# Optimization experiments

Hardware: AMD Instinct MI355X
Metric: run time of the kernel (lower is better)

Reference implementation:

```python
import jax, jax.numpy as jnp
import numpy as np

BITS = 8
NUM_HEADS = 16
EMB = 1024
MLP = 4096
BATCH = 4
SEQ = 1024


def _fq(x, bits, signed=True, narrow=False):
    """Fake-quantize with per-tensor absmax scale (brevitas MinMax/MaxStats style),
    straight-through-estimator round. signed+narrow => weight quant; signed non-narrow
    => activation quant; unsigned => QuantReLU output."""
    if signed:
        qmax = 2.0 ** (bits - 1) - 1.0
        qmin = -qmax if narrow else -(qmax + 1.0)
    else:
        qmax = 2.0 ** bits - 1.0
        qmin = 0.0
    scale = jax.lax.stop_gradient(jnp.max(jnp.abs(x)) / qmax)
    scale = jnp.maximum(scale, jnp.asarray(1e-8, x.dtype))
    q = x / scale
    q = q + jax.lax.stop_gradient(jnp.round(q) - q)  # STE round
    return jnp.clip(q, qmin, qmax) * scale


def _layernorm(x, eps=1e-5):
    mu = jnp.mean(x, axis=-1, keepdims=True)
    var = jnp.mean(jnp.square(x - mu), axis=-1, keepdims=True)
    return (x - mu) * jax.lax.rsqrt(var + eps)


def setup_inputs() -> dict:
    key = jax.random.key(0)
    ks = jax.random.split(key, 11)
    def w(k, shape, fan_in):
        return jax.random.normal(k, shape, jnp.float32) * (1.0 / np.sqrt(fan_in))
    return {
        "x": jax.random.normal(ks[0], (BATCH, SEQ, EMB), jnp.float32),
        "Wq": w(ks[1], (EMB, EMB), EMB), "bq": jnp.zeros((EMB,), jnp.float32),
        "Wk": w(ks[2], (EMB, EMB), EMB), "bk": jnp.zeros((EMB,), jnp.float32),
        "Wv": w(ks[3], (EMB, EMB), EMB), "bv": jnp.zeros((EMB,), jnp.float32),
        "Wo": w(ks[4], (EMB, EMB), EMB), "bo": jnp.zeros((EMB,), jnp.float32),
        "W1": w(ks[5], (MLP, EMB), EMB), "b1": jnp.zeros((MLP,), jnp.float32),
        "W2": w(ks[6], (EMB, MLP), MLP), "b2": jnp.zeros((EMB,), jnp.float32),
    }


def reference(x, Wq, bq, Wk, bk, Wv, bv, Wo, bo, W1, b1, W2, b2):
    B, S, E = x.shape
    H, D = NUM_HEADS, EMB // NUM_HEADS
    fqw = lambda W: _fq(W, BITS, signed=True, narrow=True)   # weight quant
    fqb = lambda b: _fq(b, BITS, signed=True)                # bias quant
    fqa = lambda a: _fq(a, BITS, signed=True)                # act quant

    # sdp_input_quant
    qx = fqa(x)
    # separate (unpacked) in-projections, torch Linear: y = x @ W.T + b
    q = qx @ fqw(Wq).T + fqb(bq)
    k = qx @ fqw(Wk).T + fqb(bk)
    v = qx @ fqw(Wv).T + fqb(bv)
    # [B,H,S,D]
    q = q.reshape(B, S, H, D).transpose(0, 2, 1, 3)
    k = k.reshape(B, S, H, D).transpose(0, 2, 1, 3)
    v = v.reshape(B, S, H, D).transpose(0, 2, 1, 3)

    q_scaled = fqa(q * (1.0 / np.sqrt(D)))          # q_scaled_quant
    k_t = fqa(k.transpose(0, 1, 3, 2))              # k_transposed_quant
    v = fqa(v)                                      # v_quant

    scores = jnp.einsum('bhqd,bhdk->bhqk', q_scaled, k_t)
    scores = fqa(scores)                            # softmax_input_quant
    attn = jax.nn.softmax(scores, axis=-1)
    attn = fqa(attn)                                # attn_output_weights_quant

    ctx = jnp.einsum('bhqk,bhkd->bhqd', attn, v)
    ctx = ctx.transpose(0, 2, 1, 3).reshape(B, S, E)
    ctx = fqa(ctx)                                  # out_proj_input_quant
    attn_out = ctx @ fqw(Wo).T + fqb(bo)

    # residual_sdp (QuantEltwiseAdd input quant on both operands) + layer-norm
    h = _layernorm(fqa(x) + fqa(attn_out))

    # MLP: QuantIdentity -> QuantLinear -> QuantReLU(unsigned) -> QuantLinear
    m = fqa(h)
    m = m @ fqw(W1).T + fqb(b1)
    m = _fq(jax.nn.relu(m), BITS, signed=False)
    m = m @ fqw(W2).T + fqb(b2)

    return _layernorm(fqa(h) + fqa(m))
```

## Files before the change

### kernel.cpp

```cpp
#include <hip/hip_runtime.h>
#include <cstdint>
#include <cstddef>

#define TB_B 4
#define TB_S 1024
#define TB_E 1024
#define TB_H 16
#define TB_D 64
#define TB_MLP 4096
#define TB_ROWS (TB_B * TB_S)

typedef int int4v __attribute__((ext_vector_type(4)));

#define LGKM0() __asm__ volatile("s_waitcnt lgkmcnt(0)" ::: "memory")
#define CMEMBAR() __asm__ volatile("" ::: "memory")

static __device__ __forceinline__ void atomicMaxF(float* addr, float v) {
  atomicMax(reinterpret_cast<unsigned int*>(addr), __float_as_uint(v));
}

static __device__ __forceinline__ float fast_exp2(float x) {
#if __has_builtin(__builtin_amdgcn_exp2f)
  return __builtin_amdgcn_exp2f(x);
#else
  return exp2f(x);
#endif
}

static __device__ __forceinline__ void gl2lds16(const void* g, void* l) {
  __builtin_amdgcn_global_load_lds(
      (const __attribute__((address_space(1))) void*)g,
      (__attribute__((address_space(3))) void*)l, 16, 0, 0);
}

struct AMDesc { const float* p; long n4; int slot; };
struct AMBatch { AMDesc d[13]; };
__global__ __launch_bounds__(256) void absmax_multi_kernel(AMBatch bt, float* ws) {
  AMDesc d = bt.d[blockIdx.y];
  float m = 0.f;
  long stride = (long)gridDim.x * 256;
  for (long i = (long)blockIdx.x * 256 + threadIdx.x; i < d.n4; i += stride) {
    float4 v = ((const float4*)d.p)[i];
    m = fmaxf(m, fmaxf(fmaxf(fabsf(v.x), fabsf(v.y)), fmaxf(fabsf(v.z), fabsf(v.w))));
  }
#pragma unroll
  for (int o = 32; o; o >>= 1) m = fmaxf(m, __shfl_down(m, o, 64));
  __shared__ float sm[4];
  if (!(threadIdx.x & 63)) sm[threadIdx.x >> 6] = m;
  __syncthreads();
  if (threadIdx.x == 0)
    atomicMaxF(ws + d.slot, fmaxf(fmaxf(sm[0], sm[1]), fmaxf(sm[2], sm[3])));
}

struct QMDesc { const float* in; signed char* out; long n4; int slot; float qmin; };
struct QMBatch { QMDesc d[7]; };
__global__ __launch_bounds__(256) void quant8_multi_kernel(QMBatch bt, const float* ws) {
  QMDesc d = bt.d[blockIdx.y];
  float scale = fmaxf(ws[d.slot] / 127.f, 1e-8f);
  long stride = (long)gridDim.x * 256;
  for (long i = (long)blockIdx.x * 256 + threadIdx.x; i < d.n4; i += stride) {
    float4 v = ((const float4*)d.in)[i];
    char4 o;
    o.x = (signed char)(int)fminf(fmaxf(rintf(v.x / scale), d.qmin), 127.f);
    o.y = (signed char)(int)fminf(fmaxf(rintf(v.y / scale), d.qmin), 127.f);
    o.z = (signed char)(int)fminf(fmaxf(rintf(v.z / scale), d.qmin), 127.f);
    o.w = (signed char)(int)fminf(fmaxf(rintf(v.w / scale), d.qmin), 127.f);
    ((char4*)d.out)[i] = o;
  }
}

struct BDesc { const float* in; float* out; int n4; int slot; };
struct BBatch { BDesc d[6]; };
__global__ __launch_bounds__(256) void bias_quant_multi_kernel(BBatch bt, const float* ws) {
  BDesc d = bt.d[blockIdx.y];
  float scale = fmaxf(ws[d.slot] / 127.f, 1e-8f);
  int i = blockIdx.x * 256 + threadIdx.x;
  if (i < d.n4) {
    float4 v = ((const float4*)d.in)[i];
    float4 o;
    o.x = fminf(fmaxf(rintf(v.x / scale), -128.f), 127.f) * scale;
    o.y = fminf(fmaxf(rintf(v.y / scale), -128.f), 127.f) * scale;
    o.z = fminf(fmaxf(rintf(v.z / scale), -128.f), 127.f) * scale;
    o.w = fminf(fmaxf(rintf(v.w / scale), -128.f), 127.f) * scale;
    ((float4*)d.out)[i] = o;
  }
}

__global__ __launch_bounds__(256) void quant8_kernel(const float* __restrict__ in,
                                                     signed char* __restrict__ out8, long n4,
                                                     const float* __restrict__ amax_p,
                                                     float pre, float qmin) {
  float scale = fmaxf(amax_p[0] * pre / 127.f, 1e-8f);
  long stride = (long)gridDim.x * 256;
  for (long i = (long)blockIdx.x * 256 + threadIdx.x; i < n4; i += stride) {
    float4 v = ((const float4*)in)[i];
    char4 o;
    o.x = (signed char)(int)fminf(fmaxf(rintf(v.x * pre / scale), qmin), 127.f);
    o.y = (signed char)(int)fminf(fmaxf(rintf(v.y * pre / scale), qmin), 127.f);
    o.z = (signed char)(int)fminf(fmaxf(rintf(v.z * pre / scale), qmin), 127.f);
    o.w = (signed char)(int)fminf(fmaxf(rintf(v.w * pre / scale), qmin), 127.f);
    ((char4*)out8)[i] = o;
  }
}

__global__ __launch_bounds__(256) void relu_quant8_kernel(const float* __restrict__ in,
                                                          signed char* __restrict__ out8, long n4,
                                                          const float* __restrict__ amax_p) {
  float scale = fmaxf(amax_p[0] / 255.f, 1e-8f);
  long stride = (long)gridDim.x * 256;
  for (long i = (long)blockIdx.x * 256 + threadIdx.x; i < n4; i += stride) {
    float4 v = ((const float4*)in)[i];
    char4 o;
    o.x = (signed char)((int)fminf(fmaxf(rintf(fmaxf(v.x, 0.f) / scale), 0.f), 255.f) - 128);
    o.y = (signed char)((int)fminf(fmaxf(rintf(fmaxf(v.y, 0.f) / scale), 0.f), 255.f) - 128);
    o.z = (signed char)((int)fminf(fmaxf(rintf(fmaxf(v.z, 0.f) / scale), 0.f), 255.f) - 128);
    o.w = (signed char)((int)fminf(fmaxf(rintf(fmaxf(v.w, 0.f) / scale), 0.f), 255.f) - 128);
    ((char4*)out8)[i] = o;
  }
}

__global__ __launch_bounds__(256) void rowsum_i8_kernel(const signed char* __restrict__ w8,
                                                        int* __restrict__ out, int Kdim) {
  const int row = blockIdx.x, t = threadIdx.x;
  const signed char* p = w8 + (long)row * Kdim;
  int s = 0;
  for (int i = t * 16; i < Kdim; i += 4096) {
    int4v v = *(const int4v*)(p + i);
    const signed char* b = (const signed char*)&v;
#pragma unroll
    for (int j = 0; j < 16; j++) s += b[j];
  }
#pragma unroll
  for (int o = 32; o; o >>= 1) s += __shfl_down(s, o, 64);
  __shared__ int sm[4];
  if (!(t & 63)) sm[t >> 6] = s;
  __syncthreads();
  if (t == 0) out[row] = sm[0] + sm[1] + sm[2] + sm[3];
}

__global__ __launch_bounds__(256) void gemm_i8_kernel(
    const signed char* __restrict__ A, const signed char* __restrict__ Bw,
    const float* __restrict__ biasq,
    const float* __restrict__ amax_a, float div_a,
    const float* __restrict__ amax_b,
    const int* __restrict__ rowsum,
    float* __restrict__ C, int M, int N, int K,
    float* __restrict__ amax_out, int relu_amax, int mode) {
  __shared__ signed char As[2][8192];
  __shared__ signed char Bs[2][8192];
  const int t = threadIdx.x;
  int bx, by;
  {
    int lin = blockIdx.y * gridDim.x + blockIdx.x;
    if ((gridDim.y & 7) == 0) {
      int xcd = lin & 7, j = lin >> 3;
      bx = j % gridDim.x;
      by = (gridDim.y >> 3) * xcd + j / gridDim.x;
    } else { bx = blockIdx.x; by = blockIdx.y; }
  }
  const int m0 = by * 128, n0 = bx * 128;
  const int w = t >> 6, lane = t & 63;
  const int fr = lane & 15, quad = lane >> 4;
  const int wm = w >> 1, wn = w & 1;
  const int r0 = t >> 2;
  const int csrc = (((t & 3) ^ ((t >> 3) & 3)) << 4);
  const int sx = ((quad ^ ((fr >> 1) & 3)) << 4);

  int4v acc[4][4];
#pragma unroll
  for (int r = 0; r < 4; r++)
#pragma unroll
    for (int c = 0; c < 4; c++) acc[r][c] = (int4v){0, 0, 0, 0};

  const long arow0 = (long)(m0 + r0) * K + csrc;
  const long arow1 = (long)(m0 + r0 + 64) * K + csrc;
  const long brow0 = (long)(n0 + r0) * K + csrc;
  const long brow1 = (long)(n0 + r0 + 64) * K + csrc;

  auto stage = [&](int buf, int kk) {
    gl2lds16(A + arow0 + kk, As[buf] + t * 16);
    gl2lds16(A + arow1 + kk, As[buf] + t * 16 + 4096);
    gl2lds16(Bw + brow0 + kk, Bs[buf] + t * 16);
    gl2lds16(Bw + brow1 + kk, Bs[buf] + t * 16 + 4096);
  };
  auto compute = [&](int buf) {
    int4v af[4], bf[4];
#pragma unroll
    for (int r = 0; r < 4; r++)
      af[r] = *(const int4v*)(As[buf] + (wm * 64 + r * 16 + fr) * 64 + sx);
#pragma unroll
    for (int c = 0; c < 4; c++)
      bf[c] = *(const int4v*)(Bs[buf] + (wn * 64 + c * 16 + fr) * 64 + sx);
#pragma unroll
    for (int r = 0; r < 4; r++)
#pragma unroll
      for (int c = 0; c < 4; c++)
        acc[r][c] = __builtin_amdgcn_mfma_i32_16x16x64_i8(af[r], bf[c], acc[r][c], 0, 0, 0);
  };

  const int nt = K >> 6;
  stage(0, 0);
  __syncthreads();
  for (int kt = 0; kt < nt; kt += 2) {
    stage(1, (kt + 1) << 6);
    compute(0);
    __syncthreads();
    if (kt + 2 < nt) stage(0, (kt + 2) << 6);
    compute(1);
    __syncthreads();
  }

  const int seg = (mode == 1) ? (n0 >> 10) : 0;
  const float s_a = fmaxf(amax_a[0] / div_a, 1e-8f);
  const float s_b = fmaxf(amax_b[seg] / 127.f, 1e-8f);
  const float s = s_a * s_b;
  float lmax = 0.f;
#pragma unroll
  for (int r = 0; r < 4; r++) {
    int rbase = m0 + wm * 64 + r * 16 + quad * 4;
#pragma unroll
    for (int c = 0; c < 4; c++) {
      int col = n0 + wn * 64 + c * 16 + fr;
      int corr = rowsum ? (rowsum[col] << 7) : 0;
      float bi = biasq[col];
      if (mode == 1) {
        int h = (col >> 6) & 15, dd = col & 63;
        float* cbase = C + (long)seg * ((long)TB_ROWS * TB_E);
#pragma unroll
        for (int g = 0; g < 4; g++) {
          int m = rbase + g;
          int b = m >> 10, sdx = m & 1023;
          float o = (float)acc[r][c][g] * s + bi;
          lmax = fmaxf(lmax, fabsf(o));
          cbase[((((long)b * TB_H + h) * TB_S) + sdx) * TB_D + dd] = o;
        }
      } else {
#pragma unroll
        for (int g = 0; g < 4; g++) {
          float o = (float)(acc[r][c][g] + corr) * s + bi;
          lmax = fmaxf(lmax, relu_amax ? fmaxf(o, 0.f) : fabsf(o));
          C[(long)(rbase + g) * N + col] = o;
        }
      }
    }
  }
#pragma unroll
  for (int o = 32; o; o >>= 1) lmax = fmaxf(lmax, __shfl_down(lmax, o, 64));
  __shared__ float redm[4];
  if (!lane) redm[w] = lmax;
  __syncthreads();
  if (t == 0) atomicMaxF(amax_out + seg, fmaxf(fmaxf(redm[0], redm[1]), fmaxf(redm[2], redm[3])));
}

__global__ __launch_bounds__(256) void quant8_vb_kernel(const float* __restrict__ v,
                                                        const float* __restrict__ amax_p,
                                                        signed char* __restrict__ v8b) {
  __shared__ signed char tile[64][80];
  const int bh = blockIdx.x;
  const int jb = blockIdx.y;
  const int s0 = jb * 64;
  const int t = threadIdx.x;
  const float scale = fmaxf(amax_p[0] / 127.f, 1e-8f);
#pragma unroll
  for (int it = 0; it < 4; it++) {
    int idx = t + it * 256;
    int r = idx >> 4, c4 = (idx & 15) * 4;
    float4 vv = *(const float4*)(v + ((long)bh * TB_S + s0 + r) * TB_D + c4);
    tile[c4 + 0][r] = (signed char)(int)fminf(fmaxf(rintf(vv.x / scale), -128.f), 127.f);
    tile[c4 + 1][r] = (signed char)(int)fminf(fmaxf(rintf(vv.y / scale), -128.f), 127.f);
    tile[c4 + 2][r] = (signed char)(int)fminf(fmaxf(rintf(vv.z / scale), -128.f), 127.f);
    tile[c4 + 3][r] = (signed char)(int)fminf(fmaxf(rintf(vv.w / scale), -128.f), 127.f);
  }
  __syncthreads();
  int d = t >> 2, sb = (t & 3) * 16;
  int4v o = *(const int4v*)&tile[d][sb];
  *(int4v*)(v8b + (((long)bh * 16 + jb) * 64 + d) * 64 + sb) = o;
}

__global__ __launch_bounds__(256) void attn_rowmax_kernel(const signed char* __restrict__ q8,
                                                          const signed char* __restrict__ k8,
                                                          int* __restrict__ irowmax,
                                                          int* __restrict__ imax_out) {
  const int bh = blockIdx.x;
  const int t = threadIdx.x, w = t >> 6, lane = t & 63;
  const int fr = lane & 15, quad = lane >> 4;
  const int i0 = blockIdx.y * 64 + w * 16;
  const long base = (long)bh * TB_S;
  int4v qf = *(const int4v*)(q8 + (base + i0 + fr) * 64 + quad * 16);
  int mx = -2147483647, mn = 2147483647;
  for (int j0 = 0; j0 < TB_S; j0 += 16) {
    int4v kf = *(const int4v*)(k8 + (base + j0 + fr) * 64 + quad * 16);
    int4v sc = __builtin_amdgcn_mfma_i32_16x16x64_i8(kf, qf, (int4v){0, 0, 0, 0}, 0, 0, 0);
    mx = max(mx, max(max(sc[0], sc[1]), max(sc[2], sc[3])));
    mn = min(mn, min(min(sc[0], sc[1]), min(sc[2], sc[3])));
  }
  mx = max(mx, __shfl_xor(mx, 16, 64));
  mx = max(mx, __shfl_xor(mx, 32, 64));
  mn = min(mn, __shfl_xor(mn, 16, 64));
  mn = min(mn, __shfl_xor(mn, 32, 64));
  if (quad == 0) irowmax[(long)bh * TB_S + i0 + fr] = mx;
  int gm = max(mx, -mn);
#pragma unroll
  for (int o = 32; o; o >>= 1) gm = max(gm, __shfl_down(gm, o, 64));
  __shared__ int sm[4];
  if (!lane) sm[w] = gm;
  __syncthreads();
  if (t == 0) atomicMax(imax_out, max(max(sm[0], sm[1]), max(sm[2], sm[3])));
}

__global__ __launch_bounds__(256) void attn_rowsum_kernel(
    const signed char* __restrict__ q8, const signed char* __restrict__ k8,
    const int* __restrict__ irowmax, const int* __restrict__ imax_p,
    const float* __restrict__ amax_q, const float* __restrict__ amax_k,
    float* __restrict__ rowl, float* __restrict__ amax_attn) {
  const int bh = blockIdx.x;
  const int t = threadIdx.x, w = t >> 6, lane = t & 63;
  const int fr = lane & 15, quad = lane >> 4;
  const int i0 = blockIdx.y * 64 + w * 16;
  const float s_q = fmaxf(amax_q[0] * 0.125f / 127.f, 1e-8f);
  const float s_k = fmaxf(amax_k[0] / 127.f, 1e-8f);
  const float sqk = s_q * s_k;
  const float s_sc = fmaxf((float)imax_p[0] * sqk / 127.f, 1e-8f);
  const float c1 = sqk / s_sc;
  const float aa = s_sc * 1.44269504088896340736f;
  const long base = (long)bh * TB_S;
  int4v qf = *(const int4v*)(q8 + (base + i0 + fr) * 64 + quad * 16);
  const int imr = irowmax[base + i0 + fr];
  const float qmax = fminf(fmaxf(rintf((float)imr * c1), -128.f), 127.f);
  const float qa = qmax * aa;
  float l = 0.f;
  for (int j0 = 0; j0 < TB_S; j0 += 16) {
    int4v kf = *(const int4v*)(k8 + (base + j0 + fr) * 64 + quad * 16);
    int4v sc = __builtin_amdgcn_mfma_i32_16x16x64_i8(kf, qf, (int4v){0, 0, 0, 0}, 0, 0, 0);
#pragma unroll
    for (int g = 0; g < 4; g++) {
      float qv = fminf(fmaxf(rintf((float)sc[g] * c1), -128.f), 127.f);
      l += fast_exp2(fmaf(qv, aa, -qa));
    }
  }
  l += __shfl_xor(l, 16, 64);
  l += __shfl_xor(l, 32, 64);
  if (quad == 0) rowl[base + i0 + fr] = l;
  float inv = 1.f / l;
#pragma unroll
  for (int o = 32; o; o >>= 1) inv = fmaxf(inv, __shfl_down(inv, o, 64));
  __shared__ float smf[4];
  if (!lane) smf[w] = inv;
  __syncthreads();
  if (t == 0) atomicMaxF(amax_attn, fmaxf(fmaxf(smf[0], smf[1]), fmaxf(smf[2], smf[3])));
}

__global__ __launch_bounds__(256) void attn_pv_kernel(
    const signed char* __restrict__ q8, const signed char* __restrict__ k8,
    const signed char* __restrict__ v8b,
    const int* __restrict__ irowmax, const int* __restrict__ imax_p,
    const float* __restrict__ amax_q, const float* __restrict__ amax_k,
    const float* __restrict__ amax_v, const float* __restrict__ amax_attn,
    const float* __restrict__ rowl,
    float* __restrict__ ctx, float* __restrict__ amax_ctx) {
  __shared__ signed char latt[4][16][80];
  const int bh = blockIdx.x, b = bh >> 4, h = bh & 15;
  const int t = threadIdx.x, w = t >> 6, lane = t & 63;
  const int fr = lane & 15, quad = lane >> 4;
  const int i0 = blockIdx.y * 64 + w * 16;
  const float s_q = fmaxf(amax_q[0] * 0.125f / 127.f, 1e-8f);
  const float s_k = fmaxf(amax_k[0] / 127.f, 1e-8f);
  const float sqk = s_q * s_k;
  const float s_sc = fmaxf((float)imax_p[0] * sqk / 127.f, 1e-8f);
  const float c1 = sqk / s_sc;
  const float aa = s_sc * 1.44269504088896340736f;
  const float s_v = fmaxf(amax_v[0] / 127.f, 1e-8f);
  const float s_at = fmaxf(amax_attn[0] / 127.f, 1e-8f);
  const long base = (long)bh * TB_S;
  int4v qf = *(const int4v*)(q8 + (base + i0 + fr) * 64 + quad * 16);
  const int imr = irowmax[base + i0 + fr];
  const float qmax = fminf(fmaxf(rintf((float)imr * c1), -128.f), 127.f);
  const float bexp = qmax * aa;
  const float li = rowl[base + i0 + fr];
  const float invls = 1.f / (li * s_at);
  int4v accv[4];
#pragma unroll
  for (int dtile = 0; dtile < 4; dtile++) accv[dtile] = (int4v){0, 0, 0, 0};

  for (int j0 = 0; j0 < TB_S; j0 += 64) {
#pragma unroll
    for (int tt = 0; tt < 4; tt++) {
      int4v kf = *(const int4v*)(k8 + (base + j0 + tt * 16 + fr) * 64 + quad * 16);
      int4v sc = __builtin_amdgcn_mfma_i32_16x16x64_i8(kf, qf, (int4v){0, 0, 0, 0}, 0, 0, 0);
      int packed = 0;
#pragma unroll
      for (int g = 0; g < 4; g++) {
        float qv = fminf(fmaxf(rintf((float)sc[g] * c1), -128.f), 127.f);
        float e = fast_exp2(fmaf(qv, aa, -bexp));
        int code = (int)fminf(fmaxf(rintf(e * invls), -128.f), 127.f);
        packed |= (code & 255) << (g * 8);
      }
      *(int*)&latt[w][fr][tt * 16 + quad * 4] = packed;
    }
    LGKM0();
    int4v af = *(const int4v*)&latt[w][fr][quad * 16];
    const signed char* vbase = v8b + (((long)bh * 16 + (j0 >> 6)) * 64) * 64;
#pragma unroll
    for (int dtile = 0; dtile < 4; dtile++) {
      int4v vf = *(const int4v*)(vbase + (dtile * 16 + fr) * 64 + quad * 16);
      accv[dtile] = __builtin_amdgcn_mfma_i32_16x16x64_i8(af, vf, accv[dtile], 0, 0, 0);
    }
    CMEMBAR();
  }
  const float sav = s_at * s_v;
  float cmax = 0.f;
#pragma unroll
  for (int dtile = 0; dtile < 4; dtile++) {
#pragma unroll
    for (int g = 0; g < 4; g++) {
      float val = (float)accv[dtile][g] * sav;
      cmax = fmaxf(cmax, fabsf(val));
      int irow = i0 + quad * 4 + g;
      ctx[(((long)(b * TB_S + irow)) * TB_H + h) * TB_D + dtile * 16 + fr] = val;
    }
  }
#pragma unroll
  for (int o = 32; o; o >>= 1) cmax = fmaxf(cmax, __shfl_down(cmax, o, 64));
  __shared__ float smf[4];
  if (!lane) smf[w] = cmax;
  __syncthreads();
  if (t == 0) atomicMaxF(amax_ctx, fmaxf(fmaxf(smf[0], smf[1]), fmaxf(smf[2], smf[3])));
}

__global__ __launch_bounds__(256) void resid_ln_kernel(const signed char* __restrict__ a8,
                                                       const float* __restrict__ amax_a,
                                                       const float* __restrict__ braw,
                                                       const float* __restrict__ amax_b,
                                                       float* __restrict__ outp,
                                                       float* __restrict__ amax_out) {
  __shared__ float red[4];
  __shared__ float redm[4];
  const int row = blockIdx.x, t = threadIdx.x;
  const float sa = fmaxf(amax_a[0] / 127.f, 1e-8f);
  const float sb = fmaxf(amax_b[0] / 127.f, 1e-8f);
  const long base = (long)row * TB_E + t * 4;
  char4 a = ((const char4*)a8)[(long)row * 256 + t];
  float4 bv = *(const float4*)(braw + base);
  float v0 = (float)a.x * sa + fminf(fmaxf(rintf(bv.x / sb), -128.f), 127.f) * sb;
  float v1 = (float)a.y * sa + fminf(fmaxf(rintf(bv.y / sb), -128.f), 127.f) * sb;
  float v2 = (float)a.z * sa + fminf(fmaxf(rintf(bv.z / sb), -128.f), 127.f) * sb;
  float v3 = (float)a.w * sa + fminf(fmaxf(rintf(bv.w / sb), -128.f), 127.f) * sb;
  float s = v0 + v1 + v2 + v3;
#pragma unroll
  for (int o = 32; o; o >>= 1) s += __shfl_down(s, o, 64);
  if (!(t & 63)) red[t >> 6] = s;
  __syncthreads();
  float mu = ((red[0] + red[1]) + (red[2] + red[3])) * (1.f / TB_E);
  float d0 = v0 - mu, d1 = v1 - mu, d2 = v2 - mu, d3 = v3 - mu;
  float sq = d0 * d0 + d1 * d1 + d2 * d2 + d3 * d3;
#pragma unroll
  for (int o = 32; o; o >>= 1) sq += __shfl_down(sq, o, 64);
  __syncthreads();
  if (!(t & 63)) red[t >> 6] = sq;
  __syncthreads();
  float var = ((red[0] + red[1]) + (red[2] + red[3])) * (1.f / TB_E);
  float rs = 1.f / sqrtf(var + 1e-5f);
  float4 o4;
  o4.x = d0 * rs; o4.y = d1 * rs; o4.z = d2 * rs; o4.w = d3 * rs;
  *(float4*)(outp + base) = o4;
  float lm = fmaxf(fmaxf(fabsf(o4.x), fabsf(o4.y)), fmaxf(fabsf(o4.z), fabsf(o4.w)));
#pragma unroll
  for (int o = 32; o; o >>= 1) lm = fmaxf(lm, __shfl_down(lm, o, 64));
  if (!(t & 63)) redm[t >> 6] = lm;
  __syncthreads();
  if (t == 0) atomicMaxF(amax_out, fmaxf(fmaxf(redm[0], redm[1]), fmaxf(redm[2], redm[3])));
}

#define SL_X 0
#define SL_WQ 1
#define SL_WK 2
#define SL_WV 3
#define SL_WO 4
#define SL_W1 5
#define SL_W2 6
#define SL_BQ 7
#define SL_BK 8
#define SL_BV 9
#define SL_BO 10
#define SL_B1 11
#define SL_B2 12
#define SL_Q 13
#define SL_K 14
#define SL_V 15
#define SL_SCI 16
#define SL_ATTN 17
#define SL_CTX 18
#define SL_AO 19
#define SL_H 20
#define SL_RELU 21
#define SL_M2 22
#define SL_DUMMY 23

static inline int nblocks(long n) {
  long b = (n + 255) / 256;
  return (int)(b > 2048 ? 2048 : b);
}

extern "C" void kernel_launch(void* const* d_in, const int* in_sizes, int n_in,
                              void* d_out, int out_size, void* d_ws, size_t ws_size,
                              hipStream_t stream) {
  const float* x  = (const float*)d_in[0];
  const float* Wq = (const float*)d_in[1];
  const float* bq = (const float*)d_in[2];
  const float* Wk = (const float*)d_in[3];
  const float* bk = (const float*)d_in[4];
  const float* Wv = (const float*)d_in[5];
  const float* bv = (const float*)d_in[6];
  const float* Wo = (const float*)d_in[7];
  const float* bo = (const float*)d_in[8];
  const float* W1 = (const float*)d_in[9];
  const float* b1 = (const float*)d_in[10];
  const float* W2 = (const float*)d_in[11];
  const float* b2 = (const float*)d_in[12];
  float* ws = (float*)d_ws;
  float* out = (float*)d_out;

  const long SZ_XE = (long)TB_ROWS * TB_E;
  const long SZ_W  = (long)TB_E * TB_E;
  const long SZ_M1 = (long)TB_ROWS * TB_MLP;

  const long OFF_QBQ = 1024, OFF_QBK = 2048, OFF_QBV = 3072, OFF_QBO = 4096;
  const long OFF_QB1 = 5120, OFF_QB2 = 9216;
  const long OFF_RSUM = 10240;
  const long OFF_Q  = 65536;
  const long OFF_K  = OFF_Q + SZ_XE;
  const long OFF_V  = OFF_K + SZ_XE;
  const long OFF_M2 = OFF_V + SZ_XE;
  const long OFF_IRM = OFF_M2 + SZ_XE;
  const long OFF_ROWL = OFF_IRM + 65536;
  const long OFF_M1 = OFF_ROWL + 65536;
  const long OFF_I8 = OFF_M1 + SZ_M1;

  float* qbuf = ws + OFF_Q;  float* kbuf = ws + OFF_K;  float* vbuf = ws + OFF_V;
  float* m2   = ws + OFF_M2;
  int*   irowmax = (int*)(ws + OFF_IRM);
  float* rowl = ws + OFF_ROWL;
  float* m1 = ws + OFF_M1;
  float* ctx = qbuf;
  float* attn_out = kbuf;
  float* hbuf = vbuf;
  float* qbq_ = ws + OFF_QBQ; float* qbk_ = ws + OFF_QBK;
  float* qbv_ = ws + OFF_QBV; float* qbo_ = ws + OFF_QBO;
  float* qb1_ = ws + OFF_QB1; float* qb2_ = ws + OFF_QB2;
  int* rsum = (int*)(ws + OFF_RSUM);
  int* imax = (int*)(ws + SL_SCI);

  signed char* i8base = (signed char*)(ws + OFF_I8);
  signed char* qx8  = i8base;
  signed char* wq8  = qx8 + SZ_XE;
  signed char* wk8  = wq8 + SZ_W;
  signed char* wv8  = wk8 + SZ_W;
  signed char* wo8  = wv8 + SZ_W;
  signed char* w18  = wo8 + SZ_W;
  signed char* w28  = w18 + SZ_XE;
  signed char* ctx8 = w28 + SZ_XE;
  signed char* m08  = ctx8 + SZ_XE;
  signed char* m18  = m08 + SZ_XE;
  signed char* q8   = m18 + SZ_M1;
  signed char* k8   = q8 + SZ_XE;
  signed char* v8b  = k8 + SZ_XE;

  hipMemsetAsync(ws, 0, 4096, stream);

  AMBatch am;
  am.d[0]  = {x,  SZ_XE/4, SL_X};
  am.d[1]  = {Wq, SZ_W/4,  SL_WQ};
  am.d[2]  = {Wk, SZ_W/4,  SL_WK};
  am.d[3]  = {Wv, SZ_W/4,  SL_WV};
  am.d[4]  = {Wo, SZ_W/4,  SL_WO};
  am.d[5]  = {W1, SZ_XE/4, SL_W1};
  am.d[6]  = {W2, SZ_XE/4, SL_W2};
  am.d[7]  = {bq, 256,     SL_BQ};
  am.d[8]  = {bk, 256,     SL_BK};
  am.d[9]  = {bv, 256,     SL_BV};
  am.d[10] = {bo, 256,     SL_BO};
  am.d[11] = {b1, 1024,    SL_B1};
  am.d[12] = {b2, 256,     SL_B2};
  absmax_multi_kernel<<<dim3(64, 13), 256, 0, stream>>>(am, ws);

  QMBatch qm;
  qm.d[0] = {x,  qx8, SZ_XE/4, SL_X,  -128.f};
  qm.d[1] = {Wq, wq8, SZ_W/4,  SL_WQ, -127.f};
  qm.d[2] = {Wk, wk8, SZ_W/4,  SL_WK, -127.f};
  qm.d[3] = {Wv, wv8, SZ_W/4,  SL_WV, -127.f};
  qm.d[4] = {W1, w18, SZ_XE/4, SL_W1, -127.f};
  qm.d[5] = {W2, w28, SZ_XE/4, SL_W2, -127.f};
  qm.d[6] = {Wo, wo8, SZ_W/4,  SL_WO, -127.f};
  quant8_multi_kernel<<<dim3(64, 7), 256, 0, stream>>>(qm, ws);
  rowsum_i8_kernel<<<TB_E, 256, 0, stream>>>(w28, rsum, TB_MLP);
  BBatch bb;
  bb.d[0] = {bq, qbq_, 256,  SL_BQ};
  bb.d[1] = {bk, qbk_, 256,  SL_BK};
  bb.d[2] = {bv, qbv_, 256,  SL_BV};
  bb.d[3] = {bo, qbo_, 256,  SL_BO};
  bb.d[4] = {b1, qb1_, 1024, SL_B1};
  bb.d[5] = {b2, qb2_, 256,  SL_B2};
  bias_quant_multi_kernel<<<dim3(4, 6), 256, 0, stream>>>(bb, ws);

  gemm_i8_kernel<<<dim3(3*TB_E/128, TB_ROWS/128), 256, 0, stream>>>(
      qx8, wq8, qbq_, ws + SL_X, 127.f, ws + SL_WQ, nullptr, qbuf,
      TB_ROWS, 3*TB_E, TB_E, ws + SL_Q, 0, 1);

  quant8_kernel<<<2048, 256, 0, stream>>>(qbuf, q8, SZ_XE/4, ws + SL_Q, 0.125f, -128.f);
  quant8_kernel<<<2048, 256, 0, stream>>>(kbuf, k8, SZ_XE/4, ws + SL_K, 1.f, -128.f);
  quant8_vb_kernel<<<dim3(TB_B*TB_H, TB_S/64), 256, 0, stream>>>(vbuf, ws + SL_V, v8b);

  attn_rowmax_kernel<<<dim3(TB_B*TB_H, TB_S/64), 256, 0, stream>>>(q8, k8, irowmax, imax);
  attn_rowsum_kernel<<<dim3(TB_B*TB_H, TB_S/64), 256, 0, stream>>>(
      q8, k8, irowmax, imax, ws + SL_Q, ws + SL_K, rowl, ws + SL_ATTN);
  attn_pv_kernel<<<dim3(TB_B*TB_H, TB_S/64), 256, 0, stream>>>(
      q8, k8, v8b, irowmax, imax, ws + SL_Q, ws + SL_K, ws + SL_V, ws + SL_ATTN,
      rowl, ctx, ws + SL_CTX);

  quant8_kernel<<<2048, 256, 0, stream>>>(ctx, ctx8, SZ_XE/4, ws + SL_CTX, 1.f, -128.f);
  gemm_i8_kernel<<<dim3(TB_E/128, TB_ROWS/128), 256, 0, stream>>>(
      ctx8, wo8, qbo_, ws + SL_CTX, 127.f, ws + SL_WO, nullptr, attn_out,
      TB_ROWS, TB_E, TB_E, ws + SL_AO, 0, 0);

  resid_ln_kernel<<<TB_ROWS, 256, 0, stream>>>(qx8, ws + SL_X, attn_out, ws + SL_AO, hbuf, ws + SL_H);

  quant8_kernel<<<2048, 256, 0, stream>>>(hbuf, m08, SZ_XE/4, ws + SL_H, 1.f, -128.f);
  gemm_i8_kernel<<<dim3(TB_MLP/128, TB_ROWS/128), 256, 0, stream>>>(
      m08, w18, qb1_, ws + SL_H, 127.f, ws + SL_W1, nullptr, m1,
      TB_ROWS, TB_MLP, TB_E, ws + SL_RELU, 1, 0);
  relu_quant8_kernel<<<nblocks(SZ_M1/4), 256, 0, stream>>>(m1, m18, SZ_M1/4, ws + SL_RELU);
  gemm_i8_kernel<<<dim3(TB_E/128, TB_ROWS/128), 256, 0, stream>>>(
      m18, w28, qb2_, ws + SL_RELU, 255.f, ws + SL_W2, rsum, m2,
      TB_ROWS, TB_E, TB_MLP, ws + SL_M2, 0, 0);

  resid_ln_kernel<<<TB_ROWS, 256, 0, stream>>>(m08, ws + SL_H, m2, ws + SL_M2, out, ws + SL_DUMMY);
}
```

Before: 551.3 us.

## Triple-buffer int8 GEMM loads and use one wave per row in layernorm

The int8 GEMM moves from a double-buffered loop with two full barriers per pair of k-tiles to a three-stage ring. It issues loads two tiles ahead, waits with a partial vmcnt, and uses a single raw barrier per tile, so global-to-LDS transfers overlap compute better. The cost is LDS use rising from 32KB to 48KB per block, which may lower occupancy. Separately, the residual-layernorm kernel now handles one row per wavefront and computes mean and variance in one pass with shuffles only, which removes the LDS reductions and barriers but uses the less numerically robust E[x^2]-mu^2 form.

Result: faster. 468.6 us (-15.0%).

```diff
diff --git a/kernel.cpp b/kernel.cpp
--- a/kernel.cpp
+++ b/kernel.cpp
@@ -14,6 +14,8 @@
 
 #define LGKM0() __asm__ volatile("s_waitcnt lgkmcnt(0)" ::: "memory")
 #define CMEMBAR() __asm__ volatile("" ::: "memory")
+#define RAW_BARRIER() do { __asm__ volatile("" ::: "memory"); \
+  __builtin_amdgcn_s_barrier(); __asm__ volatile("" ::: "memory"); } while (0)
 
 static __device__ __forceinline__ void atomicMaxF(float* addr, float v) {
   atomicMax(reinterpret_cast<unsigned int*>(addr), __float_as_uint(v));
@@ -146,8 +148,8 @@
     const int* __restrict__ rowsum,
     float* __restrict__ C, int M, int N, int K,
     float* __restrict__ amax_out, int relu_amax, int mode) {
-  __shared__ signed char As[2][8192];
-  __shared__ signed char Bs[2][8192];
+  __shared__ signed char As[3][8192];
+  __shared__ signed char Bs[3][8192];
   const int t = threadIdx.x;
   int bx, by;
   {
@@ -177,7 +179,8 @@
   const long brow0 = (long)(n0 + r0) * K + csrc;
   const long brow1 = (long)(n0 + r0 + 64) * K + csrc;
 
-  auto stage = [&](int buf, int kk) {
+  auto stage = [&](int buf, int kt) {
+    const int kk = kt << 6;
     gl2lds16(A + arow0 + kk, As[buf] + t * 16);
     gl2lds16(A + arow1 + kk, As[buf] + t * 16 + 4096);
     gl2lds16(Bw + brow0 + kk, Bs[buf] + t * 16);
@@ -200,15 +203,18 @@
 
   const int nt = K >> 6;
   stage(0, 0);
-  __syncthreads();
-  for (int kt = 0; kt < nt; kt += 2) {
-    stage(1, (kt + 1) << 6);
-    compute(0);
-    __syncthreads();
-    if (kt + 2 < nt) stage(0, (kt + 2) << 6);
-    compute(1);
-    __syncthreads();
-  }
+  stage(1, 1);
+  int cbuf = 0, sbuf = 2;
+  for (int kt = 0; kt < nt - 1; ++kt) {
+    __asm__ volatile("s_waitcnt vmcnt(4)" ::: "memory");
+    RAW_BARRIER();
+    if (kt + 2 < nt) { stage(sbuf, kt + 2); sbuf = (sbuf == 2) ? 0 : sbuf + 1; }
+    compute(cbuf);
+    cbuf = (cbuf == 2) ? 0 : cbuf + 1;
+  }
+  __asm__ volatile("s_waitcnt vmcnt(0)" ::: "memory");
+  RAW_BARRIER();
+  compute(cbuf);
 
   const int seg = (mode == 1) ? (n0 >> 10) : 0;
   const float s_a = fmaxf(amax_a[0] / div_a, 1e-8f);
@@ -433,40 +439,48 @@
                                                        const float* __restrict__ amax_b,
                                                        float* __restrict__ outp,
                                                        float* __restrict__ amax_out) {
-  __shared__ float red[4];
-  __shared__ float redm[4];
-  const int row = blockIdx.x, t = threadIdx.x;
+  const int t = threadIdx.x, w = t >> 6, lane = t & 63;
+  const int row = blockIdx.x * 4 + w;
   const float sa = fmaxf(amax_a[0] / 127.f, 1e-8f);
   const float sb = fmaxf(amax_b[0] / 127.f, 1e-8f);
-  const long base = (long)row * TB_E + t * 4;
-  char4 a = ((const char4*)a8)[(long)row * 256 + t];
-  float4 bv = *(const float4*)(braw + base);
-  float v0 = (float)a.x * sa + fminf(fmaxf(rintf(bv.x / sb), -128.f), 127.f) * sb;
-  float v1 = (float)a.y * sa + fminf(fmaxf(rintf(bv.y / sb), -128.f), 127.f) * sb;
-  float v2 = (float)a.z * sa + fminf(fmaxf(rintf(bv.z / sb), -128.f), 127.f) * sb;
-  float v3 = (float)a.w * sa + fminf(fmaxf(rintf(bv.w / sb), -128.f), 127.f) * sb;
-  float s = v0 + v1 + v2 + v3;
-#pragma unroll
-  for (int o = 32; o; o >>= 1) s += __shfl_down(s, o, 64);
-  if (!(t & 63)) red[t >> 6] = s;
-  __syncthreads();
-  float mu = ((red[0] + red[1]) + (red[2] + red[3])) * (1.f / TB_E);
-  float d0 = v0 - mu, d1 = v1 - mu, d2 = v2 - mu, d3 = v3 - mu;
-  float sq = d0 * d0 + d1 * d1 + d2 * d2 + d3 * d3;
-#pragma unroll
-  for (int o = 32; o; o >>= 1) sq += __shfl_down(sq, o, 64);
-  __syncthreads();
-  if (!(t & 63)) red[t >> 6] = sq;
-  __syncthreads();
-  float var = ((red[0] + red[1]) + (red[2] + red[3])) * (1.f / TB_E);
-  float rs = 1.f / sqrtf(var + 1e-5f);
-  float4 o4;
-  o4.x = d0 * rs; o4.y = d1 * rs; o4.z = d2 * rs; o4.w = d3 * rs;
-  *(float4*)(outp + base) = o4;
-  float lm = fmaxf(fmaxf(fabsf(o4.x), fabsf(o4.y)), fmaxf(fabsf(o4.z), fabsf(o4.w)));
+  const long base = (long)row * TB_E;
+  float v[16];
+  float s = 0.f, q = 0.f;
+#pragma unroll
+  for (int j = 0; j < 4; j++) {
+    char4 a = ((const char4*)(a8 + base))[j * 64 + lane];
+    float4 bv = *(const float4*)(braw + base + j * 256 + lane * 4);
+    float x0 = (float)a.x * sa + fminf(fmaxf(rintf(bv.x / sb), -128.f), 127.f) * sb;
+    float x1 = (float)a.y * sa + fminf(fmaxf(rintf(bv.y / sb), -128.f), 127.f) * sb;
+    float x2 = (float)a.z * sa + fminf(fmaxf(rintf(bv.z / sb), -128.f), 127.f) * sb;
+    float x3 = (float)a.w * sa + fminf(fmaxf(rintf(bv.w / sb), -128.f), 127.f) * sb;
+    v[j * 4 + 0] = x0; v[j * 4 + 1] = x1; v[j * 4 + 2] = x2; v[j * 4 + 3] = x3;
+    s += (x0 + x1) + (x2 + x3);
+    q += (x0 * x0 + x1 * x1) + (x2 * x2 + x3 * x3);
+  }
+#pragma unroll
+  for (int o = 32; o; o >>= 1) {
+    s += __shfl_xor(s, o, 64);
+    q += __shfl_xor(q, o, 64);
+  }
+  const float mu = s * (1.f / TB_E);
+  const float var = fmaxf(q * (1.f / TB_E) - mu * mu, 0.f);
+  const float rs = 1.f / sqrtf(var + 1e-5f);
+  float lm = 0.f;
+#pragma unroll
+  for (int j = 0; j < 4; j++) {
+    float4 o4;
+    o4.x = (v[j * 4 + 0] - mu) * rs;
+    o4.y = (v[j * 4 + 1] - mu) * rs;
+    o4.z = (v[j * 4 + 2] - mu) * rs;
+    o4.w = (v[j * 4 + 3] - mu) * rs;
+    *(float4*)(outp + base + j * 256 + lane * 4) = o4;
+    lm = fmaxf(lm, fmaxf(fmaxf(fabsf(o4.x), fabsf(o4.y)), fmaxf(fabsf(o4.z), fabsf(o4.w))));
+  }
 #pragma unroll
   for (int o = 32; o; o >>= 1) lm = fmaxf(lm, __shfl_down(lm, o, 64));
-  if (!(t & 63)) redm[t >> 6] = lm;
+  __shared__ float redm[4];
+  if (!lane) redm[w] = lm;
   __syncthreads();
   if (t == 0) atomicMaxF(amax_out, fmaxf(fmaxf(redm[0], redm[1]), fmaxf(redm[2], redm[3])));
 }
@@ -622,7 +636,7 @@
       ctx8, wo8, qbo_, ws + SL_CTX, 127.f, ws + SL_WO, nullptr, attn_out,
       TB_ROWS, TB_E, TB_E, ws + SL_AO, 0, 0);
 
-  resid_ln_kernel<<<TB_ROWS, 256, 0, stream>>>(qx8, ws + SL_X, attn_out, ws + SL_AO, hbuf, ws + SL_H);
+  resid_ln_kernel<<<TB_ROWS/4, 256, 0, stream>>>(qx8, ws + SL_X, attn_out, ws + SL_AO, hbuf, ws + SL_H);
 
   quant8_kernel<<<2048, 256, 0, stream>>>(hbuf, m08, SZ_XE/4, ws + SL_H, 1.f, -128.f);
   gemm_i8_kernel<<<dim3(TB_MLP/128, TB_ROWS/128), 256, 0, stream>>>(
@@ -633,5 +647,5 @@
       m18, w28, qb2_, ws + SL_RELU, 255.f, ws + SL_W2, rsum, m2,
       TB_ROWS, TB_E, TB_MLP, ws + SL_M2, 0, 0);
 
-  resid_ln_kernel<<<TB_ROWS, 256, 0, stream>>>(m08, ws + SL_H, m2, ws + SL_M2, out, ws + SL_DUMMY);
-}
+  resid_ln_kernel<<<TB_ROWS/4, 256, 0, stream>>>(m08, ws + SL_H, m2, ws + SL_M2, out, ws + SL_DUMMY);
+}
```
